# Performance work log

Measured on AMD Instinct MI355X. Metric: run time of the kernel, lower is better.

Reference implementation:

```python
import jax, jax.numpy as jnp
import numpy as np

B, L, D, F = 4096, 200, 64, 100000


def setup_inputs() -> dict:
    key = jax.random.key(0)
    ks = jax.random.split(key, 12)
    film_hist = jax.random.randint(ks[0], (B, L), 0, F)                 # padded rated-film indices
    ratings = jax.random.uniform(ks[1], (B, L), jnp.float32) * 4.5 + 0.5  # letterboxd-style 0.5..5
    lengths = jax.random.randint(ks[2], (B,), 1, L + 1)                 # ragged history lengths (>=1)
    film_indices = jax.random.randint(ks[3], (B,), 0, F)                # target films to score
    emb_table = jax.random.normal(ks[4], (F, D), jnp.float32) * 0.1
    W1 = jax.random.normal(ks[5], (5 * D, 2 * D), jnp.float32) * 0.05
    b1 = jnp.zeros((2 * D,), jnp.float32)
    W2 = jax.random.normal(ks[6], (2 * D, D), jnp.float32) * 0.05
    b2 = jnp.zeros((D,), jnp.float32)
    W3 = jax.random.normal(ks[7], (D, 1), jnp.float32) * 0.05
    b3 = jnp.zeros((1,), jnp.float32)
    return {"film_hist": film_hist, "ratings": ratings, "lengths": lengths,
            "film_indices": film_indices, "emb_table": emb_table,
            "W1": W1, "b1": b1, "W2": W2, "b2": b2, "W3": W3, "b3": b3}


def _user_embeddings(film_hist, ratings, lengths, emb_table):
    # mask[b, l] = l < lengths[b]
    mask = jnp.arange(L)[None, :] < lengths[:, None]          # [B, L]
    n = lengths.astype(jnp.float32)                           # [B]
    mean_r = jnp.sum(jnp.where(mask, ratings, 0.0), axis=1) / n
    weights = ratings - mean_r[:, None] + 0.1                 # [B, L]
    hist_emb = emb_table[film_hist]                           # [B, L, D]
    w = hist_emb * weights[:, :, None]                        # weighted film embeddings
    m3 = mask[:, :, None]
    wmin = jnp.min(jnp.where(m3, w, jnp.inf), axis=1)
    wmax = jnp.max(jnp.where(m3, w, -jnp.inf), axis=1)
    wmean = jnp.sum(jnp.where(m3, w, 0.0), axis=1) / n[:, None]
    # median: sort valid entries (pads go to +inf at the end); torch.median
    # returns the lower middle element -> index (n-1)//2
    ws = jnp.sort(jnp.where(m3, w, jnp.inf), axis=1)
    mid = ((lengths - 1) // 2)[:, None, None]                 # [B,1,1]
    wmed = jnp.take_along_axis(ws, jnp.broadcast_to(mid, (B, 1, D)), axis=1)[:, 0, :]
    ue = jnp.concatenate([wmin, wmax, wmean, wmed], axis=1)   # [B, 4D]
    return ue / jnp.linalg.norm(ue, axis=1, keepdims=True)


def reference(film_hist, ratings, lengths, film_indices, emb_table, W1, b1, W2, b2, W3, b3):
    ue = _user_embeddings(film_hist, ratings, lengths, emb_table)  # [B, 4D]
    fe = emb_table[film_indices]                                   # [B, D]
    x = jnp.concatenate([ue, fe], axis=1)                          # [B, 5D]
    h = jax.nn.relu(x @ W1 + b1)   # Dropout(0.2) is identity in eval
    h = jax.nn.relu(h @ W2 + b2)
    return jax.nn.sigmoid(h @ W3 + b3)[:, 0]                       # [B]
```

## Files before the change

### kernel.cpp

```cpp
#include <hip/hip_runtime.h>
#include <hip/hip_bf16.h>
#include <stdint.h>


#define B_ 4096
#define L_ 200
#define D_ 64
#define LPAD 224

__global__ __launch_bounds__(512) void fused_kernel(
    const int* __restrict__ film_hist,
    const float* __restrict__ ratings,
    const int* __restrict__ lengths,
    const int* __restrict__ film_indices,
    const float* __restrict__ emb,
    const float* __restrict__ W1, const float* __restrict__ b1,
    const float* __restrict__ W2, const float* __restrict__ b2,
    const float* __restrict__ W3, const float* __restrict__ b3,
    float* __restrict__ out)
{
  __shared__ int   hist_s[LPAD];
  __shared__ float rat_s[LPAD];
  __shared__ float red[8];
  __shared__ float ue[4*D_];
  __shared__ float xls[320];
  __shared__ float ph[512];
  __shared__ float h1s[128];
  __shared__ float h2s[64];

  const int b = blockIdx.x;
  const int t = threadIdx.x;
  const int wave = t >> 6;
  const int lane = t & 63;
  const int sub  = lane >> 3;
  const int dloc = lane & 7;
  const int d    = wave * 8 + dloc;
  const int n = lengths[b];
  const int cmax  = (n + 7) >> 3;
  const int cmax4 = (cmax + 3) & ~3;

  float r = 0.f;
  if (t < n) {
    hist_s[t] = film_hist[(size_t)b*L_ + t];
    float rv = ratings[(size_t)b*L_ + t];
    rat_s[t] = rv; r = rv;
  }
  if (t >= 448) {
    int fi = film_indices[b];
    xls[256 + (t-448)] = emb[(size_t)fi*D_ + (t-448)];
  }

  float s = r;
  #pragma unroll
  for (int off = 32; off; off >>= 1) s += __shfl_down(s, off);
  if (lane == 0) red[wave] = s;
  __syncthreads();
  const float mean_r = (red[0]+red[1]+red[2]+red[3]+red[4]+red[5]+red[6]+red[7]) / (float)n;
  const float mr1 = 0.1f - mean_r;

  for (int l = n + t; l < 8*cmax4; l += 512) {
    hist_s[l] = hist_s[n-1];
    rat_s[l]  = rat_s[n-1];
  }
  __syncthreads();

  float vmin = __builtin_inff(), vmax = -__builtin_inff(), vsum = 0.f;
  uint32_t W[16];
  #pragma unroll
  for (int i = 0; i < 16; ++i) W[i] = 0u;

  const float* embd = emb + d;
  float vb[2][4], rb[2][4];
  {
    #pragma unroll
    for (int j = 0; j < 4; ++j) {
      const int l = sub + 8*j;
      rb[0][j] = rat_s[l];
      vb[0][j] = embd[(size_t)hist_s[l] * D_];
    }
  }
  #pragma unroll
  for (int ch = 0; ch < 7; ++ch) {
    const int cur = ch & 1, nxt = cur ^ 1;
    if ((ch+1)*4 < cmax4) {
      #pragma unroll
      for (int j = 0; j < 4; ++j) {
        const int l = sub + 8*((ch+1)*4 + j);
        rb[nxt][j] = rat_s[l];
        vb[nxt][j] = embd[(size_t)hist_s[l] * D_];
      }
    }
    if (ch*4 < cmax4) {
      uint32_t kk[4];
      #pragma unroll
      for (int j = 0; j < 4; ++j) {
        const int l = sub + 8*(ch*4 + j);
        const float w = vb[cur][j] * (rb[cur][j] + mr1);
        vmin = fminf(vmin, w); vmax = fmaxf(vmax, w);
        vsum += (l < n) ? w : 0.f;
        uint32_t u = __float_as_uint(w);
        kk[j] = (u ^ (0x80000000u | (uint32_t)((int32_t)u >> 31))) >> 16;
      }
      W[2*ch]   = kk[0] | (kk[1] << 16);
      W[2*ch+1] = kk[2] | (kk[3] << 16);
    }
  }

  vmin = fminf(vmin, __shfl_xor(vmin, 8));
  vmin = fminf(vmin, __shfl_xor(vmin, 16));
  vmin = fminf(vmin, __shfl_xor(vmin, 32));
  vmax = fmaxf(vmax, __shfl_xor(vmax, 8));
  vmax = fmaxf(vmax, __shfl_xor(vmax, 16));
  vmax = fmaxf(vmax, __shfl_xor(vmax, 32));
  vsum += __shfl_xor(vsum, 8);
  vsum += __shfl_xor(vsum, 16);
  vsum += __shfl_xor(vsum, 32);

  #define XS(k, jj, m) { uint32_t tt = ((W[k] ^ (W[(k)|(jj)] >> (jj))) & (m)); \
                         W[k] ^= tt; W[(k)|(jj)] ^= (tt << (jj)); }
  XS(0,8,0x00FF00FFu) XS(1,8,0x00FF00FFu) XS(2,8,0x00FF00FFu) XS(3,8,0x00FF00FFu)
  XS(4,8,0x00FF00FFu) XS(5,8,0x00FF00FFu) XS(6,8,0x00FF00FFu) XS(7,8,0x00FF00FFu)
  XS(0,4,0x0F0F0F0Fu) XS(1,4,0x0F0F0F0Fu) XS(2,4,0x0F0F0F0Fu) XS(3,4,0x0F0F0F0Fu)
  XS(8,4,0x0F0F0F0Fu) XS(9,4,0x0F0F0F0Fu) XS(10,4,0x0F0F0F0Fu) XS(11,4,0x0F0F0F0Fu)
  XS(0,2,0x33333333u) XS(1,2,0x33333333u) XS(4,2,0x33333333u) XS(5,2,0x33333333u)
  XS(8,2,0x33333333u) XS(9,2,0x33333333u) XS(12,2,0x33333333u) XS(13,2,0x33333333u)
  XS(0,1,0x55555555u) XS(2,1,0x55555555u) XS(4,1,0x55555555u) XS(6,1,0x55555555u)
  XS(8,1,0x55555555u) XS(10,1,0x55555555u) XS(12,1,0x55555555u) XS(14,1,0x55555555u)
  #undef XS

  const int c  = (n - sub + 7) >> 3;
  const int ce = (c + 1) >> 1, cf = c >> 1;
  uint32_t alive = ((1u << ce) - 1u) << (16 - ce);
  if (cf) alive |= ((1u << cf) - 1u) << (32 - cf);
  int k = (n - 1) >> 1;
  uint32_t prefix = 0;
  #pragma unroll
  for (int bb = 15; bb >= 0; --bb) {
    const uint32_t P = W[15 - bb];
    uint32_t z = alive & ~P;
    int cnt = __popc(z);
    cnt += __shfl_xor(cnt, 8);
    cnt += __shfl_xor(cnt, 16);
    cnt += __shfl_xor(cnt, 32);
    const bool zs = (k < cnt);
    alive  = zs ? z : (alive & P);
    k      = zs ? k : (k - cnt);
    prefix = zs ? prefix : (prefix | (1u << bb));
  }

  if (sub == 0) {
    uint32_t key32 = (prefix << 16) | 0x8000u;
    float med = (prefix & 0x8000u) ? __uint_as_float(key32 ^ 0x80000000u)
                                   : __uint_as_float(~key32);
    ue[d]      = vmin;
    ue[64 + d] = vmax;
    ue[128+ d] = vsum / (float)n;
    ue[192+ d] = med;
  }
  __syncthreads();

  float v = (t < 256) ? ue[t] : 0.f;
  float ss = v*v;
  #pragma unroll
  for (int off = 32; off; off >>= 1) ss += __shfl_down(ss, off);
  if (lane == 0) red[wave] = ss;
  __syncthreads();
  const float rn2 = 1.0f / sqrtf(red[0]+red[1]+red[2]+red[3]+red[4]+red[5]+red[6]+red[7]);
  if (t < 256) xls[t] = v * rn2;
  __syncthreads();

  {
    const int j = t & 127, q = t >> 7;
    const float* Wp = W1 + (size_t)(q*80)*128 + j;
    const float* xp = xls + q*80;
    float a0 = 0.f, a1 = 0.f;
    #pragma unroll 8
    for (int i = 0; i < 80; i += 2) {
      a0 += xp[i]   * Wp[(size_t)i*128];
      a1 += xp[i+1] * Wp[(size_t)(i+1)*128];
    }
    ph[t] = a0 + a1;
  }
  __syncthreads();
  if (t < 128) h1s[t] = fmaxf(b1[t] + ph[t] + ph[t+128] + ph[t+256] + ph[t+384], 0.f);
  __syncthreads();

  {
    const int j = t & 63, q = t >> 6;
    const float* Wp = W2 + (size_t)(q*16)*64 + j;
    const float* hp = h1s + q*16;
    float a = 0.f;
    #pragma unroll
    for (int i = 0; i < 16; ++i) a += hp[i] * Wp[(size_t)i*64];
    ph[t] = a;
  }
  __syncthreads();
  if (t < 64) {
    float h = b2[t] + ph[t] + ph[t+64] + ph[t+128] + ph[t+192]
                    + ph[t+256] + ph[t+320] + ph[t+384] + ph[t+448];
    h2s[t] = fmaxf(h, 0.f);
  }
  __syncthreads();

  if (t < 64) {
    float vv = h2s[t] * W3[t];
    #pragma unroll
    for (int off = 32; off; off >>= 1) vv += __shfl_down(vv, off);
    if (t == 0) out[b] = 1.f / (1.f + __expf(-(vv + b3[0])));
  }
}

extern "C" void kernel_launch(void* const* d_in, const int* in_sizes, int n_in,
                              void* d_out, int out_size, void* d_ws, size_t ws_size,
                              hipStream_t stream) {
  const int*   film_hist = (const int*)d_in[0];
  const float* ratings   = (const float*)d_in[1];
  const int*   lengths   = (const int*)d_in[2];
  const int*   film_idx  = (const int*)d_in[3];
  const float* emb       = (const float*)d_in[4];
  const float* W1 = (const float*)d_in[5];
  const float* b1 = (const float*)d_in[6];
  const float* W2 = (const float*)d_in[7];
  const float* b2 = (const float*)d_in[8];
  const float* W3 = (const float*)d_in[9];
  const float* b3 = (const float*)d_in[10];

  fused_kernel<<<B_, 512, 0, stream>>>(film_hist, ratings, lengths, film_idx, emb,
                                       W1, b1, W2, b2, W3, b3, (float*)d_out);
}
```

Before: 61.01 us.

## Gather embedding rows coalesced and transpose median keys through shared memory

```diff
diff --git a/kernel.cpp b/kernel.cpp
--- a/kernel.cpp
+++ b/kernel.cpp
@@ -7,6 +7,7 @@
 #define L_ 200
 #define D_ 64
 #define LPAD 224
+#define KP_U16 228
 
 __global__ __launch_bounds__(512) void fused_kernel(
     const int* __restrict__ film_hist,
@@ -24,17 +25,16 @@
   __shared__ float red[8];
   __shared__ float ue[4*D_];
   __shared__ float xls[320];
-  __shared__ float ph[512];
-  __shared__ float h1s[128];
-  __shared__ float h2s[64];
+  __shared__ float red3[3*512];
+  __shared__ union {
+    uint16_t keys[D_*KP_U16];
+    struct { float ph[512]; float h1s[128]; float h2s[64]; } m;
+  } sh;
 
   const int b = blockIdx.x;
   const int t = threadIdx.x;
-  const int wave = t >> 6;
+  const int w = t >> 6;
   const int lane = t & 63;
-  const int sub  = lane >> 3;
-  const int dloc = lane & 7;
-  const int d    = wave * 8 + dloc;
   const int n = lengths[b];
   const int cmax  = (n + 7) >> 3;
   const int cmax4 = (cmax + 3) & ~3;
@@ -53,7 +53,7 @@
   float s = r;
   #pragma unroll
   for (int off = 32; off; off >>= 1) s += __shfl_down(s, off);
-  if (lane == 0) red[wave] = s;
+  if (lane == 0) red[w] = s;
   __syncthreads();
   const float mean_r = (red[0]+red[1]+red[2]+red[3]+red[4]+red[5]+red[6]+red[7]) / (float)n;
   const float mr1 = 0.1f - mean_r;
@@ -65,56 +65,65 @@
   __syncthreads();
 
   float vmin = __builtin_inff(), vmax = -__builtin_inff(), vsum = 0.f;
-  uint32_t W[16];
-  #pragma unroll
-  for (int i = 0; i < 16; ++i) W[i] = 0u;
-
-  const float* embd = emb + d;
-  float vb[2][4], rb[2][4];
-  {
-    #pragma unroll
-    for (int j = 0; j < 4; ++j) {
-      const int l = sub + 8*j;
-      rb[0][j] = rat_s[l];
-      vb[0][j] = embd[(size_t)hist_s[l] * D_];
-    }
-  }
+  uint16_t* kout = sh.keys + lane*KP_U16 + w*28;
   #pragma unroll
   for (int ch = 0; ch < 7; ++ch) {
-    const int cur = ch & 1, nxt = cur ^ 1;
-    if ((ch+1)*4 < cmax4) {
+    if (ch*4 < cmax4) {
+      float vv[4], wg[4];
+      int   ll[4];
+      #pragma unroll
+      for (int j = 0; j < 4; ++j) ll[j] = w + 8*(ch*4 + j);
+      #pragma unroll
+      for (int j = 0; j < 4; ++j) vv[j] = emb[(size_t)hist_s[ll[j]]*D_ + lane];
+      #pragma unroll
+      for (int j = 0; j < 4; ++j) wg[j] = rat_s[ll[j]] + mr1;
+      uint32_t kk[4];
       #pragma unroll
       for (int j = 0; j < 4; ++j) {
-        const int l = sub + 8*((ch+1)*4 + j);
-        rb[nxt][j] = rat_s[l];
-        vb[nxt][j] = embd[(size_t)hist_s[l] * D_];
-      }
-    }
-    if (ch*4 < cmax4) {
-      uint32_t kk[4];
-      #pragma unroll
-      for (int j = 0; j < 4; ++j) {
-        const int l = sub + 8*(ch*4 + j);
-        const float w = vb[cur][j] * (rb[cur][j] + mr1);
-        vmin = fminf(vmin, w); vmax = fmaxf(vmax, w);
-        vsum += (l < n) ? w : 0.f;
-        uint32_t u = __float_as_uint(w);
+        const float wv = vv[j] * wg[j];
+        vmin = fminf(vmin, wv); vmax = fmaxf(vmax, wv);
+        vsum += (ll[j] < n) ? wv : 0.f;
+        uint32_t u = __float_as_uint(wv);
         kk[j] = (u ^ (0x80000000u | (uint32_t)((int32_t)u >> 31))) >> 16;
       }
-      W[2*ch]   = kk[0] | (kk[1] << 16);
-      W[2*ch+1] = kk[2] | (kk[3] << 16);
+      uint2 pr;
+      pr.x = kk[0] | (kk[1] << 16);
+      pr.y = kk[2] | (kk[3] << 16);
+      *(uint2*)(kout + ch*4) = pr;
     }
   }
-
-  vmin = fminf(vmin, __shfl_xor(vmin, 8));
-  vmin = fminf(vmin, __shfl_xor(vmin, 16));
-  vmin = fminf(vmin, __shfl_xor(vmin, 32));
-  vmax = fmaxf(vmax, __shfl_xor(vmax, 8));
-  vmax = fmaxf(vmax, __shfl_xor(vmax, 16));
-  vmax = fmaxf(vmax, __shfl_xor(vmax, 32));
-  vsum += __shfl_xor(vsum, 8);
-  vsum += __shfl_xor(vsum, 16);
-  vsum += __shfl_xor(vsum, 32);
+  red3[t] = vmin; red3[512 + t] = vmax; red3[1024 + t] = vsum;
+  __syncthreads();
+
+  if (t < 64) {
+    float m = red3[t];
+    #pragma unroll
+    for (int ww = 1; ww < 8; ++ww) m = fminf(m, red3[ww*64 + t]);
+    ue[t] = m;
+  } else if (t < 128) {
+    const int dd = t - 64;
+    float m = red3[512 + dd];
+    #pragma unroll
+    for (int ww = 1; ww < 8; ++ww) m = fmaxf(m, red3[512 + ww*64 + dd]);
+    ue[64 + dd] = m;
+  } else if (t < 192) {
+    const int dd = t - 128;
+    float m = red3[1024 + dd];
+    #pragma unroll
+    for (int ww = 1; ww < 8; ++ww) m += red3[1024 + ww*64 + dd];
+    ue[128 + dd] = m / (float)n;
+  }
+
+  const int sub  = lane >> 3;
+  const int dsel = w*8 + (lane & 7);
+  const uint16_t* kp = sh.keys + dsel*KP_U16 + sub*28;
+  uint32_t W[16];
+  #pragma unroll
+  for (int i = 0; i < 7; ++i) {
+    uint2 v = *(const uint2*)(kp + 4*i);
+    W[2*i] = v.x; W[2*i+1] = v.y;
+  }
+  W[14] = 0u; W[15] = 0u;
 
   #define XS(k, jj, m) { uint32_t tt = ((W[k] ^ (W[(k)|(jj)] >> (jj))) & (m)); \
                          W[k] ^= tt; W[(k)|(jj)] ^= (tt << (jj)); }
@@ -147,15 +156,11 @@
     k      = zs ? k : (k - cnt);
     prefix = zs ? prefix : (prefix | (1u << bb));
   }
-
   if (sub == 0) {
     uint32_t key32 = (prefix << 16) | 0x8000u;
     float med = (prefix & 0x8000u) ? __uint_as_float(key32 ^ 0x80000000u)
                                    : __uint_as_float(~key32);
-    ue[d]      = vmin;
-    ue[64 + d] = vmax;
-    ue[128+ d] = vsum / (float)n;
-    ue[192+ d] = med;
+    ue[192 + dsel] = med;
   }
   __syncthreads();
 
@@ -163,7 +168,7 @@
   float ss = v*v;
   #pragma unroll
   for (int off = 32; off; off >>= 1) ss += __shfl_down(ss, off);
-  if (lane == 0) red[wave] = ss;
+  if (lane == 0) red[w] = ss;
   __syncthreads();
   const float rn2 = 1.0f / sqrtf(red[0]+red[1]+red[2]+red[3]+red[4]+red[5]+red[6]+red[7]);
   if (t < 256) xls[t] = v * rn2;
@@ -179,31 +184,32 @@
       a0 += xp[i]   * Wp[(size_t)i*128];
       a1 += xp[i+1] * Wp[(size_t)(i+1)*128];
     }
-    ph[t] = a0 + a1;
-  }
-  __syncthreads();
-  if (t < 128) h1s[t] = fmaxf(b1[t] + ph[t] + ph[t+128] + ph[t+256] + ph[t+384], 0.f);
+    sh.m.ph[t] = a0 + a1;
+  }
+  __syncthreads();
+  if (t < 128) sh.m.h1s[t] = fmaxf(b1[t] + sh.m.ph[t] + sh.m.ph[t+128]
+                                         + sh.m.ph[t+256] + sh.m.ph[t+384], 0.f);
   __syncthreads();
 
   {
     const int j = t & 63, q = t >> 6;
     const float* Wp = W2 + (size_t)(q*16)*64 + j;
-    const float* hp = h1s + q*16;
+    const float* hp = sh.m.h1s + q*16;
     float a = 0.f;
     #pragma unroll
     for (int i = 0; i < 16; ++i) a += hp[i] * Wp[(size_t)i*64];
-    ph[t] = a;
+    sh.m.ph[t] = a;
   }
   __syncthreads();
   if (t < 64) {
-    float h = b2[t] + ph[t] + ph[t+64] + ph[t+128] + ph[t+192]
-                    + ph[t+256] + ph[t+320] + ph[t+384] + ph[t+448];
-    h2s[t] = fmaxf(h, 0.f);
+    float h = b2[t] + sh.m.ph[t] + sh.m.ph[t+64] + sh.m.ph[t+128] + sh.m.ph[t+192]
+                    + sh.m.ph[t+256] + sh.m.ph[t+320] + sh.m.ph[t+384] + sh.m.ph[t+448];
+    sh.m.h2s[t] = fmaxf(h, 0.f);
   }
   __syncthreads();
 
   if (t < 64) {
-    float vv = h2s[t] * W3[t];
+    float vv = sh.m.h2s[t] * W3[t];
     #pragma unroll
     for (int off = 32; off; off >>= 1) vv += __shfl_down(vv, off);
     if (t == 0) out[b] = 1.f / (1.f + __expf(-(vv + b3[0])));
```

After: 61.69 us. Within noise of the previous version (+1.1%).

## Process two users per block to share MLP weight loads

Applied to the files above, without the earlier changes.

```diff
diff --git a/kernel.cpp b/kernel.cpp
--- a/kernel.cpp
+++ b/kernel.cpp
@@ -7,6 +7,107 @@
 #define L_ 200
 #define D_ 64
 #define LPAD 224
+
+__device__ __forceinline__ void user_pass(
+    const float* __restrict__ emb,
+    const int* hist_s, const float* rat_s,
+    const int n, const float mr1, float* xrow,
+    const int lane, const int sub, const int d)
+{
+  const int cmax  = (n + 7) >> 3;
+  const int cmax4 = (cmax + 3) & ~3;
+
+  float vmin = __builtin_inff(), vmax = -__builtin_inff(), vsum = 0.f;
+  uint32_t W[16];
+  #pragma unroll
+  for (int i = 0; i < 16; ++i) W[i] = 0u;
+
+  const float* embd = emb + d;
+  float vb[2][4], rb[2][4];
+  #pragma unroll
+  for (int j = 0; j < 4; ++j) {
+    const int l = sub + 8*j;
+    rb[0][j] = rat_s[l];
+    vb[0][j] = embd[(size_t)hist_s[l] * D_];
+  }
+  #pragma unroll
+  for (int ch = 0; ch < 7; ++ch) {
+    const int cur = ch & 1, nxt = cur ^ 1;
+    if ((ch+1)*4 < cmax4) {
+      #pragma unroll
+      for (int j = 0; j < 4; ++j) {
+        const int l = sub + 8*((ch+1)*4 + j);
+        rb[nxt][j] = rat_s[l];
+        vb[nxt][j] = embd[(size_t)hist_s[l] * D_];
+      }
+    }
+    if (ch*4 < cmax4) {
+      uint32_t kk[4];
+      #pragma unroll
+      for (int j = 0; j < 4; ++j) {
+        const int l = sub + 8*(ch*4 + j);
+        const float wv = vb[cur][j] * (rb[cur][j] + mr1);
+        vmin = fminf(vmin, wv); vmax = fmaxf(vmax, wv);
+        vsum += (l < n) ? wv : 0.f;
+        uint32_t u = __float_as_uint(wv);
+        kk[j] = (u ^ (0x80000000u | (uint32_t)((int32_t)u >> 31))) >> 16;
+      }
+      W[2*ch]   = kk[0] | (kk[1] << 16);
+      W[2*ch+1] = kk[2] | (kk[3] << 16);
+    }
+  }
+
+  vmin = fminf(vmin, __shfl_xor(vmin, 8));
+  vmin = fminf(vmin, __shfl_xor(vmin, 16));
+  vmin = fminf(vmin, __shfl_xor(vmin, 32));
+  vmax = fmaxf(vmax, __shfl_xor(vmax, 8));
+  vmax = fmaxf(vmax, __shfl_xor(vmax, 16));
+  vmax = fmaxf(vmax, __shfl_xor(vmax, 32));
+  vsum += __shfl_xor(vsum, 8);
+  vsum += __shfl_xor(vsum, 16);
+  vsum += __shfl_xor(vsum, 32);
+
+  #define XS(k, jj, m) { uint32_t tt = ((W[k] ^ (W[(k)|(jj)] >> (jj))) & (m)); \
+                         W[k] ^= tt; W[(k)|(jj)] ^= (tt << (jj)); }
+  XS(0,8,0x00FF00FFu) XS(1,8,0x00FF00FFu) XS(2,8,0x00FF00FFu) XS(3,8,0x00FF00FFu)
+  XS(4,8,0x00FF00FFu) XS(5,8,0x00FF00FFu) XS(6,8,0x00FF00FFu) XS(7,8,0x00FF00FFu)
+  XS(0,4,0x0F0F0F0Fu) XS(1,4,0x0F0F0F0Fu) XS(2,4,0x0F0F0F0Fu) XS(3,4,0x0F0F0F0Fu)
+  XS(8,4,0x0F0F0F0Fu) XS(9,4,0x0F0F0F0Fu) XS(10,4,0x0F0F0F0Fu) XS(11,4,0x0F0F0F0Fu)
+  XS(0,2,0x33333333u) XS(1,2,0x33333333u) XS(4,2,0x33333333u) XS(5,2,0x33333333u)
+  XS(8,2,0x33333333u) XS(9,2,0x33333333u) XS(12,2,0x33333333u) XS(13,2,0x33333333u)
+  XS(0,1,0x55555555u) XS(2,1,0x55555555u) XS(4,1,0x55555555u) XS(6,1,0x55555555u)
+  XS(8,1,0x55555555u) XS(10,1,0x55555555u) XS(12,1,0x55555555u) XS(14,1,0x55555555u)
+  #undef XS
+
+  const int c  = (n - sub + 7) >> 3;
+  const int ce = (c + 1) >> 1, cf = c >> 1;
+  uint32_t alive = ((1u << ce) - 1u) << (16 - ce);
+  if (cf) alive |= ((1u << cf) - 1u) << (32 - cf);
+  int k = (n - 1) >> 1;
+  uint32_t prefix = 0;
+  #pragma unroll
+  for (int bb = 15; bb >= 0; --bb) {
+    const uint32_t P = W[15 - bb];
+    uint32_t z = alive & ~P;
+    int cnt = __popc(z);
+    cnt += __shfl_xor(cnt, 8);
+    cnt += __shfl_xor(cnt, 16);
+    cnt += __shfl_xor(cnt, 32);
+    const bool zs = (k < cnt);
+    alive  = zs ? z : (alive & P);
+    k      = zs ? k : (k - cnt);
+    prefix = zs ? prefix : (prefix | (1u << bb));
+  }
+  if (sub == 0) {
+    uint32_t key32 = (prefix << 16) | 0x8000u;
+    float med = (prefix & 0x8000u) ? __uint_as_float(key32 ^ 0x80000000u)
+                                   : __uint_as_float(~key32);
+    xrow[d]       = vmin;
+    xrow[64 + d]  = vmax;
+    xrow[128 + d] = vsum / (float)n;
+    xrow[192 + d] = med;
+  }
+}
 
 __global__ __launch_bounds__(512) void fused_kernel(
     const int* __restrict__ film_hist,
@@ -19,194 +120,119 @@
     const float* __restrict__ W3, const float* __restrict__ b3,
     float* __restrict__ out)
 {
-  __shared__ int   hist_s[LPAD];
-  __shared__ float rat_s[LPAD];
+  __shared__ int   hist_s[2][LPAD];
+  __shared__ float rat_s[2][LPAD];
   __shared__ float red[8];
-  __shared__ float ue[4*D_];
-  __shared__ float xls[320];
-  __shared__ float ph[512];
-  __shared__ float h1s[128];
-  __shared__ float h2s[64];
-
-  const int b = blockIdx.x;
+  __shared__ float xraw[2][320];
+  __shared__ float ph[1024];
+  __shared__ float h1s[2][128];
+
   const int t = threadIdx.x;
-  const int wave = t >> 6;
+  const int w = t >> 6;
   const int lane = t & 63;
   const int sub  = lane >> 3;
-  const int dloc = lane & 7;
-  const int d    = wave * 8 + dloc;
-  const int n = lengths[b];
-  const int cmax  = (n + 7) >> 3;
-  const int cmax4 = (cmax + 3) & ~3;
-
-  float r = 0.f;
-  if (t < n) {
-    hist_s[t] = film_hist[(size_t)b*L_ + t];
-    float rv = ratings[(size_t)b*L_ + t];
-    rat_s[t] = rv; r = rv;
-  }
-  if (t >= 448) {
-    int fi = film_indices[b];
-    xls[256 + (t-448)] = emb[(size_t)fi*D_ + (t-448)];
-  }
-
-  float s = r;
-  #pragma unroll
-  for (int off = 32; off; off >>= 1) s += __shfl_down(s, off);
-  if (lane == 0) red[wave] = s;
-  __syncthreads();
-  const float mean_r = (red[0]+red[1]+red[2]+red[3]+red[4]+red[5]+red[6]+red[7]) / (float)n;
-  const float mr1 = 0.1f - mean_r;
-
-  for (int l = n + t; l < 8*cmax4; l += 512) {
-    hist_s[l] = hist_s[n-1];
-    rat_s[l]  = rat_s[n-1];
-  }
-  __syncthreads();
-
-  float vmin = __builtin_inff(), vmax = -__builtin_inff(), vsum = 0.f;
-  uint32_t W[16];
-  #pragma unroll
-  for (int i = 0; i < 16; ++i) W[i] = 0u;
-
-  const float* embd = emb + d;
-  float vb[2][4], rb[2][4];
-  {
-    #pragma unroll
-    for (int j = 0; j < 4; ++j) {
-      const int l = sub + 8*j;
-      rb[0][j] = rat_s[l];
-      vb[0][j] = embd[(size_t)hist_s[l] * D_];
-    }
-  }
-  #pragma unroll
-  for (int ch = 0; ch < 7; ++ch) {
-    const int cur = ch & 1, nxt = cur ^ 1;
-    if ((ch+1)*4 < cmax4) {
-      #pragma unroll
-      for (int j = 0; j < 4; ++j) {
-        const int l = sub + 8*((ch+1)*4 + j);
-        rb[nxt][j] = rat_s[l];
-        vb[nxt][j] = embd[(size_t)hist_s[l] * D_];
-      }
-    }
-    if (ch*4 < cmax4) {
-      uint32_t kk[4];
-      #pragma unroll
-      for (int j = 0; j < 4; ++j) {
-        const int l = sub + 8*(ch*4 + j);
-        const float w = vb[cur][j] * (rb[cur][j] + mr1);
-        vmin = fminf(vmin, w); vmax = fmaxf(vmax, w);
-        vsum += (l < n) ? w : 0.f;
-        uint32_t u = __float_as_uint(w);
-        kk[j] = (u ^ (0x80000000u | (uint32_t)((int32_t)u >> 31))) >> 16;
-      }
-      W[2*ch]   = kk[0] | (kk[1] << 16);
-      W[2*ch+1] = kk[2] | (kk[3] << 16);
-    }
-  }
-
-  vmin = fminf(vmin, __shfl_xor(vmin, 8));
-  vmin = fminf(vmin, __shfl_xor(vmin, 16));
-  vmin = fminf(vmin, __shfl_xor(vmin, 32));
-  vmax = fmaxf(vmax, __shfl_xor(vmax, 8));
-  vmax = fmaxf(vmax, __shfl_xor(vmax, 16));
-  vmax = fmaxf(vmax, __shfl_xor(vmax, 32));
-  vsum += __shfl_xor(vsum, 8);
-  vsum += __shfl_xor(vsum, 16);
-  vsum += __shfl_xor(vsum, 32);
-
-  #define XS(k, jj, m) { uint32_t tt = ((W[k] ^ (W[(k)|(jj)] >> (jj))) & (m)); \
-                         W[k] ^= tt; W[(k)|(jj)] ^= (tt << (jj)); }
-  XS(0,8,0x00FF00FFu) XS(1,8,0x00FF00FFu) XS(2,8,0x00FF00FFu) XS(3,8,0x00FF00FFu)
-  XS(4,8,0x00FF00FFu) XS(5,8,0x00FF00FFu) XS(6,8,0x00FF00FFu) XS(7,8,0x00FF00FFu)
-  XS(0,4,0x0F0F0F0Fu) XS(1,4,0x0F0F0F0Fu) XS(2,4,0x0F0F0F0Fu) XS(3,4,0x0F0F0F0Fu)
-  XS(8,4,0x0F0F0F0Fu) XS(9,4,0x0F0F0F0Fu) XS(10,4,0x0F0F0F0Fu) XS(11,4,0x0F0F0F0Fu)
-  XS(0,2,0x33333333u) XS(1,2,0x33333333u) XS(4,2,0x33333333u) XS(5,2,0x33333333u)
-  XS(8,2,0x33333333u) XS(9,2,0x33333333u) XS(12,2,0x33333333u) XS(13,2,0x33333333u)
-  XS(0,1,0x55555555u) XS(2,1,0x55555555u) XS(4,1,0x55555555u) XS(6,1,0x55555555u)
-  XS(8,1,0x55555555u) XS(10,1,0x55555555u) XS(12,1,0x55555555u) XS(14,1,0x55555555u)
-  #undef XS
-
-  const int c  = (n - sub + 7) >> 3;
-  const int ce = (c + 1) >> 1, cf = c >> 1;
-  uint32_t alive = ((1u << ce) - 1u) << (16 - ce);
-  if (cf) alive |= ((1u << cf) - 1u) << (32 - cf);
-  int k = (n - 1) >> 1;
-  uint32_t prefix = 0;
-  #pragma unroll
-  for (int bb = 15; bb >= 0; --bb) {
-    const uint32_t P = W[15 - bb];
-    uint32_t z = alive & ~P;
-    int cnt = __popc(z);
-    cnt += __shfl_xor(cnt, 8);
-    cnt += __shfl_xor(cnt, 16);
-    cnt += __shfl_xor(cnt, 32);
-    const bool zs = (k < cnt);
-    alive  = zs ? z : (alive & P);
-    k      = zs ? k : (k - cnt);
-    prefix = zs ? prefix : (prefix | (1u << bb));
-  }
-
-  if (sub == 0) {
-    uint32_t key32 = (prefix << 16) | 0x8000u;
-    float med = (prefix & 0x8000u) ? __uint_as_float(key32 ^ 0x80000000u)
-                                   : __uint_as_float(~key32);
-    ue[d]      = vmin;
-    ue[64 + d] = vmax;
-    ue[128+ d] = vsum / (float)n;
-    ue[192+ d] = med;
-  }
-  __syncthreads();
-
-  float v = (t < 256) ? ue[t] : 0.f;
-  float ss = v*v;
-  #pragma unroll
-  for (int off = 32; off; off >>= 1) ss += __shfl_down(ss, off);
-  if (lane == 0) red[wave] = ss;
-  __syncthreads();
-  const float rn2 = 1.0f / sqrtf(red[0]+red[1]+red[2]+red[3]+red[4]+red[5]+red[6]+red[7]);
-  if (t < 256) xls[t] = v * rn2;
-  __syncthreads();
-
-  {
-    const int j = t & 127, q = t >> 7;
-    const float* Wp = W1 + (size_t)(q*80)*128 + j;
-    const float* xp = xls + q*80;
-    float a0 = 0.f, a1 = 0.f;
-    #pragma unroll 8
-    for (int i = 0; i < 80; i += 2) {
-      a0 += xp[i]   * Wp[(size_t)i*128];
-      a1 += xp[i+1] * Wp[(size_t)(i+1)*128];
-    }
-    ph[t] = a0 + a1;
-  }
-  __syncthreads();
-  if (t < 128) h1s[t] = fmaxf(b1[t] + ph[t] + ph[t+128] + ph[t+256] + ph[t+384], 0.f);
-  __syncthreads();
-
-  {
-    const int j = t & 63, q = t >> 6;
-    const float* Wp = W2 + (size_t)(q*16)*64 + j;
-    const float* hp = h1s + q*16;
-    float a = 0.f;
-    #pragma unroll
-    for (int i = 0; i < 16; ++i) a += hp[i] * Wp[(size_t)i*64];
-    ph[t] = a;
-  }
-  __syncthreads();
-  if (t < 64) {
-    float h = b2[t] + ph[t] + ph[t+64] + ph[t+128] + ph[t+192]
-                    + ph[t+256] + ph[t+320] + ph[t+384] + ph[t+448];
-    h2s[t] = fmaxf(h, 0.f);
-  }
-  __syncthreads();
-
-  if (t < 64) {
-    float vv = h2s[t] * W3[t];
+  const int d    = w*8 + (lane & 7);
+  const int bA = 2*blockIdx.x, bB = bA + 1;
+  const int nA = lengths[bA], nB = lengths[bB];
+
+  {
+    const int u  = t >> 8;
+    const int tt = t & 255;
+    const int nu = u ? nB : nA;
+    float r = 0.f;
+    if (tt < LPAD) {
+      const int bu = bA + u;
+      const int idx = (tt < nu) ? tt : (nu - 1);
+      hist_s[u][tt] = film_hist[(size_t)bu*L_ + idx];
+      float rv = ratings[(size_t)bu*L_ + idx];
+      rat_s[u][tt] = rv;
+      r = (tt < nu) ? rv : 0.f;
+    }
+    if (t >= 448) {
+      const int dd = t - 448;
+      xraw[0][256+dd] = emb[(size_t)film_indices[bA]*D_ + dd];
+      xraw[1][256+dd] = emb[(size_t)film_indices[bB]*D_ + dd];
+    }
+    float s = r;
+    #pragma unroll
+    for (int off = 32; off; off >>= 1) s += __shfl_down(s, off);
+    if (lane == 0) red[w] = s;
+  }
+  __syncthreads();
+  const float mr1A = 0.1f - (red[0]+red[1]+red[2]+red[3]) / (float)nA;
+  const float mr1B = 0.1f - (red[4]+red[5]+red[6]+red[7]) / (float)nB;
+
+  user_pass(emb, hist_s[0], rat_s[0], nA, mr1A, xraw[0], lane, sub, d);
+  user_pass(emb, hist_s[1], rat_s[1], nB, mr1B, xraw[1], lane, sub, d);
+  __syncthreads();
+
+  {
+    const int u  = t >> 8;
+    const int tt = t & 255;
+    float v = xraw[u][tt];
+    float ss = v*v;
+    #pragma unroll
+    for (int off = 32; off; off >>= 1) ss += __shfl_down(ss, off);
+    if (lane == 0) red[w] = ss;
+    __syncthreads();
+    const float rn = 1.0f / sqrtf(u ? (red[4]+red[5]+red[6]+red[7])
+                                    : (red[0]+red[1]+red[2]+red[3]));
+    xraw[u][tt] = v * rn;
+  }
+  __syncthreads();
+
+  {
+    const int j = t & 127, g = t >> 7;
+    const float* Wp = W1 + (size_t)(g*80)*128 + j;
+    const float* xa = xraw[0] + g*80;
+    const float* xb = xraw[1] + g*80;
+    float aA = 0.f, aB = 0.f;
+    #pragma unroll 4
+    for (int i = 0; i < 80; ++i) {
+      const float wv = Wp[(size_t)i*128];
+      aA += wv * xa[i];
+      aB += wv * xb[i];
+    }
+    ph[g*256 + j]       = aA;
+    ph[g*256 + 128 + j] = aB;
+  }
+  __syncthreads();
+
+  if (t < 256) {
+    const int u = t >> 7, j = t & 127;
+    const float h = b1[j] + ph[u*128 + j] + ph[256 + u*128 + j]
+                          + ph[512 + u*128 + j] + ph[768 + u*128 + j];
+    h1s[u][j] = fmaxf(h, 0.f);
+  }
+  __syncthreads();
+
+  {
+    const int j = t & 63, g = t >> 6;
+    const float* Wp = W2 + (size_t)(g*16)*64 + j;
+    const float* ha = h1s[0] + g*16;
+    const float* hb = h1s[1] + g*16;
+    float aA = 0.f, aB = 0.f;
+    #pragma unroll
+    for (int i = 0; i < 16; ++i) {
+      const float wv = Wp[(size_t)i*64];
+      aA += wv * ha[i];
+      aB += wv * hb[i];
+    }
+    ph[g*128 + j]      = aA;
+    ph[g*128 + 64 + j] = aB;
+  }
+  __syncthreads();
+
+  if (t < 128) {
+    const int u = t >> 6, j = t & 63;
+    float h = b2[j];
+    #pragma unroll
+    for (int g = 0; g < 8; ++g) h += ph[g*128 + u*64 + j];
+    h = fmaxf(h, 0.f);
+    float vv = h * W3[j];
     #pragma unroll
     for (int off = 32; off; off >>= 1) vv += __shfl_down(vv, off);
-    if (t == 0) out[b] = 1.f / (1.f + __expf(-(vv + b3[0])));
+    if (j == 0) out[bA + u] = 1.f / (1.f + __expf(-(vv + b3[0])));
   }
 }
 
@@ -225,6 +251,6 @@
   const float* W3 = (const float*)d_in[9];
   const float* b3 = (const float*)d_in[10];
 
-  fused_kernel<<<B_, 512, 0, stream>>>(film_hist, ratings, lengths, film_idx, emb,
-                                       W1, b1, W2, b2, W3, b3, (float*)d_out);
+  fused_kernel<<<B_/2, 512, 0, stream>>>(film_hist, ratings, lengths, film_idx, emb,
+                                         W1, b1, W2, b2, W3, b3, (float*)d_out);
 }
```

Result: no change. 60.51 us (-0.8%).
